# Kernel tuning notes

Hardware: AMD Instinct MI355X
Metric: run time of the kernel (lower is better)

Reference implementation:

```python
import jax, jax.numpy as jnp
import numpy as np

BS, SEQ, NV, DM, K = 128, 2048, 64, 512, 64
MAX_ITER, TOL = 10, 1e-4


def setup_inputs() -> dict:
    key = jax.random.key(0)
    k1, k2, k3, k4 = jax.random.split(key, 4)
    x = jax.random.normal(k1, (BS, SEQ, NV), jnp.float32)
    bound = 1.0 / np.sqrt(SEQ)
    W = jax.random.uniform(k2, (DM, SEQ), jnp.float32, -bound, bound)  # nn.Linear weight
    b = jax.random.uniform(k3, (DM,), jnp.float32, -bound, bound)
    centroids = jax.random.normal(k4, (K, DM), jnp.float32)  # kaiming-uniform-init param (random stand-in)
    return {"x": x, "W": W, "b": b, "centroids": centroids}


def _kmeans(x_emb, centroids):
    # x_emb: [N, DM]; fixed-length scan with a `done` flag emulating torch's tol break.
    N = x_emb.shape[0]
    x_sq = jnp.sum(x_emb * x_emb, axis=1, keepdims=True)  # [N,1]

    def body(state, _):
        cent, ids, done = state
        # squared euclidean distances (argmin-equivalent to cdist p=2)
        d2 = x_sq - 2.0 * (x_emb @ cent.T) + jnp.sum(cent * cent, axis=1)  # [N,K]
        new_ids = jnp.argmin(d2, axis=1)
        sums = jax.ops.segment_sum(x_emb, new_ids, num_segments=K)          # [K,DM]
        counts = jax.ops.segment_sum(jnp.ones((N,), x_emb.dtype), new_ids, num_segments=K)
        means = sums / jnp.maximum(counts, 1.0)[:, None]
        new_cent = jnp.where((counts > 0)[:, None], means, cent)  # empty cluster keeps old centroid
        shift = jnp.linalg.norm(new_cent - cent)
        cent_out = jnp.where(done, cent, new_cent)
        ids_out = jnp.where(done, ids, new_ids)
        done_out = done | (shift < TOL)
        return (cent_out, ids_out, done_out), None

    init = (centroids, jnp.zeros((N,), jnp.int32), jnp.array(False))
    (cent, ids, _), _ = jax.lax.scan(body, init, None, length=MAX_ITER)
    return ids, cent


def reference(x, W, b, centroids):
    # x: [bs, seq, n_vars] -> permute -> linear(seq->d_model) -> [bs*n_vars, d_model]
    xt = jnp.transpose(x, (0, 2, 1))                 # [bs, n_vars, seq]
    x_emb = (xt @ W.T + b).reshape(-1, DM)           # [bs*n_vars, d_model]
    ids, cent = _kmeans(x_emb, centroids)
    prob = jax.nn.one_hot(ids, K, dtype=jnp.float32).reshape(BS, NV, K)
    return prob, cent, x_emb
```

## Files before the change

### kernel.cpp

```cpp
#include <hip/hip_runtime.h>

#define SEQ 2048
#define NVAR 64
#define DMODEL 512
#define BSZ 128
#define KC 64
#define NPT (BSZ*NVAR)
#define MAXIT 10

typedef __bf16 bf16x8 __attribute__((ext_vector_type(8)));
typedef float f32x4 __attribute__((ext_vector_type(4)));

__device__ __forceinline__ void load_lds16(const void* g, void* l) {
  __builtin_amdgcn_global_load_lds((const __attribute__((address_space(1))) void*)g,
                                   (__attribute__((address_space(3))) void*)l, 16, 0, 0);
}

__device__ __forceinline__ unsigned short bf16_rn(float x) {
  unsigned int u = __float_as_uint(x);
  u += 0x7fffu + ((u >> 16) & 1u);
  return (unsigned short)(u >> 16);
}

__global__ __launch_bounds__(256) void init_k(const float* __restrict__ c0,
    float* __restrict__ cent, unsigned short* __restrict__ centh,
    unsigned short* __restrict__ centl, float* __restrict__ csq4,
    int* __restrict__ done, float* __restrict__ shift2, int* __restrict__ ticket) {
  const int k = blockIdx.x, t = threadIdx.x;
  __shared__ float red[256];
  float v0, v1;
  {
    int d = t;
    v0 = c0[k * DMODEL + d];
    cent[k * DMODEL + d] = v0;
    unsigned short h = bf16_rn(v0);
    centh[k * DMODEL + d] = h;
    centl[k * DMODEL + d] = bf16_rn(v0 - __uint_as_float((unsigned)h << 16));
  }
  {
    int d = t + 256;
    v1 = c0[k * DMODEL + d];
    cent[k * DMODEL + d] = v1;
    unsigned short h = bf16_rn(v1);
    centh[k * DMODEL + d] = h;
    centl[k * DMODEL + d] = bf16_rn(v1 - __uint_as_float((unsigned)h << 16));
  }
  red[t] = v0 * v0; __syncthreads();
  for (int s = 64; s > 0; s >>= 1) { if ((t & 127) < s) red[t] += red[t + s]; __syncthreads(); }
  if (t == 0)   csq4[0 * KC + k] = red[0];
  if (t == 128) csq4[1 * KC + k] = red[128];
  __syncthreads();
  red[t] = v1 * v1; __syncthreads();
  for (int s = 64; s > 0; s >>= 1) { if ((t & 127) < s) red[t] += red[t + s]; __syncthreads(); }
  if (t == 0)   csq4[2 * KC + k] = red[0];
  if (t == 128) csq4[3 * KC + k] = red[128];
  if (k == 0 && t < MAXIT) { shift2[t] = 0.f; ticket[t] = 0; }
  if (k == 0 && t == 31) *done = 0;
}

__global__ __launch_bounds__(256) void conv_w(const float* __restrict__ W,
    unsigned short* __restrict__ Wh, unsigned short* __restrict__ Wl) {
  int i = (blockIdx.x * 256 + threadIdx.x) * 4;
  float4 v = *(const float4*)(W + i);
  ushort4 h, l;
  h.x = bf16_rn(v.x); l.x = bf16_rn(v.x - __uint_as_float((unsigned)h.x << 16));
  h.y = bf16_rn(v.y); l.y = bf16_rn(v.y - __uint_as_float((unsigned)h.y << 16));
  h.z = bf16_rn(v.z); l.z = bf16_rn(v.z - __uint_as_float((unsigned)h.z << 16));
  h.w = bf16_rn(v.w); l.w = bf16_rn(v.w - __uint_as_float((unsigned)h.w << 16));
  *(ushort4*)(Wh + i) = h;
  *(ushort4*)(Wl + i) = l;
}

__global__ __launch_bounds__(256) void conv_x(const float* __restrict__ x,
    unsigned short* __restrict__ Xh, unsigned short* __restrict__ Xl) {
  __shared__ float tile[64 * 65];
  const int k0 = blockIdx.x * 64;
  const int bs = blockIdx.y;
  const int t = threadIdx.x;
  const float* xb = x + (size_t)bs * SEQ * NVAR + (size_t)k0 * NVAR;
  #pragma unroll
  for (int p = 0; p < 4; ++p) {
    int idx = t + 256 * p;
    int row = idx >> 4, c4 = (idx & 15) * 4;
    float4 v = *(const float4*)(xb + row * NVAR + c4);
    tile[row * 65 + c4 + 0] = v.x; tile[row * 65 + c4 + 1] = v.y;
    tile[row * 65 + c4 + 2] = v.z; tile[row * 65 + c4 + 3] = v.w;
  }
  __syncthreads();
  const int v = t >> 2;
  const int kc = (t & 3) * 16;
  unsigned short h[16], l[16];
  #pragma unroll
  for (int j = 0; j < 16; ++j) {
    float f = tile[(kc + j) * 65 + v];
    h[j] = bf16_rn(f);
    l[j] = bf16_rn(f - __uint_as_float((unsigned)h[j] << 16));
  }
  size_t off = (size_t)(bs * 64 + v) * SEQ + k0 + kc;
  *(uint4*)(Xh + off)     = *(uint4*)&h[0];
  *(uint4*)(Xh + off + 8) = *(uint4*)&h[8];
  *(uint4*)(Xl + off)     = *(uint4*)&l[0];
  *(uint4*)(Xl + off + 8) = *(uint4*)&l[8];
}

__global__ __launch_bounds__(256) void gemm_mfma(
    const unsigned short* __restrict__ Ah, const unsigned short* __restrict__ Al,
    const unsigned short* __restrict__ Bh, const unsigned short* __restrict__ Bl,
    const float* __restrict__ bias, float* __restrict__ emb) {
  __shared__ unsigned short sAh[32 * 64] __attribute__((aligned(16)));
  __shared__ unsigned short sAl[32 * 64] __attribute__((aligned(16)));
  __shared__ unsigned short sBh[256 * 64] __attribute__((aligned(16)));
  __shared__ unsigned short sBl[256 * 64] __attribute__((aligned(16)));
  const int t = threadIdx.x;
  const int w = t >> 6, lane = t & 63;
  const int m0 = blockIdx.x * 32;
  const int n0 = blockIdx.y * 256;
  const int wn = w * 64;
  const int lrow = lane >> 3, sl8 = lane & 7;
  const int csrc = sl8 ^ lrow;

  f32x4 acc[2][4];
  #pragma unroll
  for (int i = 0; i < 2; ++i)
    #pragma unroll
    for (int j = 0; j < 4; ++j) acc[i][j] = (f32x4){0.f, 0.f, 0.f, 0.f};

  for (int kt = 0; kt < SEQ; kt += 64) {
    __syncthreads();
    {
      const int r = w * 8 + lrow;
      const size_t ga = (size_t)(m0 + r) * SEQ + kt + csrc * 8;
      load_lds16(Ah + ga, &sAh[r * 64 + sl8 * 8]);
      load_lds16(Al + ga, &sAl[r * 64 + sl8 * 8]);
    }
    #pragma unroll
    for (int i = 0; i < 8; ++i) {
      const int r = w * 64 + i * 8 + lrow;
      const size_t gb = (size_t)(n0 + r) * SEQ + kt + csrc * 8;
      load_lds16(Bh + gb, &sBh[r * 64 + sl8 * 8]);
      load_lds16(Bl + gb, &sBl[r * 64 + sl8 * 8]);
    }
    __syncthreads();
    #pragma unroll
    for (int kk = 0; kk < 2; ++kk) {
      const int sl = ((kk * 4 + (lane >> 4)) ^ (lane & 7)) * 8;
      bf16x8 ah[2], al[2], bh[4], bl[4];
      #pragma unroll
      for (int mi = 0; mi < 2; ++mi) {
        int off = (mi * 16 + (lane & 15)) * 64 + sl;
        ah[mi] = *(const bf16x8*)&sAh[off];
        al[mi] = *(const bf16x8*)&sAl[off];
      }
      #pragma unroll
      for (int ni = 0; ni < 4; ++ni) {
        int off = (wn + ni * 16 + (lane & 15)) * 64 + sl;
        bh[ni] = *(const bf16x8*)&sBh[off];
        bl[ni] = *(const bf16x8*)&sBl[off];
      }
      #pragma unroll
      for (int mi = 0; mi < 2; ++mi)
        #pragma unroll
        for (int ni = 0; ni < 4; ++ni) {
          acc[mi][ni] = __builtin_amdgcn_mfma_f32_16x16x32_bf16(ah[mi], bh[ni], acc[mi][ni], 0, 0, 0);
          acc[mi][ni] = __builtin_amdgcn_mfma_f32_16x16x32_bf16(ah[mi], bl[ni], acc[mi][ni], 0, 0, 0);
          acc[mi][ni] = __builtin_amdgcn_mfma_f32_16x16x32_bf16(al[mi], bh[ni], acc[mi][ni], 0, 0, 0);
        }
    }
  }
  #pragma unroll
  for (int ni = 0; ni < 4; ++ni) {
    const int n = n0 + wn + ni * 16 + (lane & 15);
    const float bv = bias[n];
    #pragma unroll
    for (int mi = 0; mi < 2; ++mi) {
      const int m = m0 + mi * 16 + (lane >> 4) * 4;
      #pragma unroll
      for (int r = 0; r < 4; ++r)
        emb[(size_t)(m + r) * DMODEL + n] = acc[mi][ni][r] + bv;
    }
  }
}

__global__ __launch_bounds__(256) void gemm_emb(const float* __restrict__ x,
    const float* __restrict__ W, const float* __restrict__ bias,
    float* __restrict__ emb) {
  __shared__ float As[64][64];
  __shared__ float Ws[64][132];
  const int bs = blockIdx.y;
  const int n0 = blockIdx.x * 128;
  const int t = threadIdx.x;
  const int tx = t & 15, ty = t >> 4;
  float bv[8];
  #pragma unroll
  for (int j = 0; j < 8; ++j) bv[j] = bias[n0 + 8 * tx + j];
  float acc[4][8];
  #pragma unroll
  for (int i = 0; i < 4; ++i)
    #pragma unroll
    for (int j = 0; j < 8; ++j) acc[i][j] = 0.f;
  const float* xb = x + (size_t)bs * SEQ * NVAR;
  for (int k0 = 0; k0 < SEQ; k0 += 64) {
    __syncthreads();
    {
      const float4* src = (const float4*)(xb + (size_t)k0 * NVAR);
      float4* dst = (float4*)&As[0][0];
      #pragma unroll
      for (int r = 0; r < 4; ++r) dst[t + 256 * r] = src[t + 256 * r];
    }
    #pragma unroll
    for (int r = 0; r < 8; ++r) {
      int idx = t + 256 * r;
      int k4 = idx & 15, n = idx >> 4;
      float4 wv = *(const float4*)(W + (size_t)(n0 + n) * SEQ + k0 + 4 * k4);
      Ws[4 * k4 + 0][n] = wv.x; Ws[4 * k4 + 1][n] = wv.y;
      Ws[4 * k4 + 2][n] = wv.z; Ws[4 * k4 + 3][n] = wv.w;
    }
    __syncthreads();
    #pragma unroll 8
    for (int kk = 0; kk < 64; ++kk) {
      const float4 a  = *(const float4*)&As[kk][4 * ty];
      const float4 w0 = *(const float4*)&Ws[kk][8 * tx];
      const float4 w1 = *(const float4*)&Ws[kk][8 * tx + 4];
      const float av[4] = {a.x, a.y, a.z, a.w};
      const float wv[8] = {w0.x, w0.y, w0.z, w0.w, w1.x, w1.y, w1.z, w1.w};
      #pragma unroll
      for (int i = 0; i < 4; ++i)
        #pragma unroll
        for (int j = 0; j < 8; ++j)
          acc[i][j] = fmaf(av[i], wv[j], acc[i][j]);
    }
  }
  #pragma unroll
  for (int i = 0; i < 4; ++i) {
    int row = bs * NVAR + 4 * ty + i;
    float4 o0 = make_float4(acc[i][0] + bv[0], acc[i][1] + bv[1],
                            acc[i][2] + bv[2], acc[i][3] + bv[3]);
    float4 o1 = make_float4(acc[i][4] + bv[4], acc[i][5] + bv[5],
                            acc[i][6] + bv[6], acc[i][7] + bv[7]);
    *(float4*)(emb + (size_t)row * DMODEL + n0 + 8 * tx) = o0;
    *(float4*)(emb + (size_t)row * DMODEL + n0 + 8 * tx + 4) = o1;
  }
}

__global__ __launch_bounds__(256) void conv_et(const float* __restrict__ emb,
    unsigned short* __restrict__ Eh, unsigned short* __restrict__ El,
    unsigned short* __restrict__ Eth, unsigned short* __restrict__ Etl) {
  __shared__ unsigned short Lh[64][72];
  __shared__ unsigned short Ll[64][72];
  const int d0 = blockIdx.x * 64;
  const int p0 = blockIdx.y * 64;
  const int t = threadIdx.x;
  #pragma unroll
  for (int q = 0; q < 2; ++q) {
    int idx = t + 256 * q;
    int r = idx >> 3, c = idx & 7;
    const float* src = emb + (size_t)(p0 + r) * DMODEL + d0 + c * 8;
    float4 v0 = *(const float4*)src;
    float4 v1 = *(const float4*)(src + 4);
    unsigned short h[8], l[8];
    const float vv[8] = {v0.x, v0.y, v0.z, v0.w, v1.x, v1.y, v1.z, v1.w};
    #pragma unroll
    for (int j = 0; j < 8; ++j) {
      h[j] = bf16_rn(vv[j]);
      l[j] = bf16_rn(vv[j] - __uint_as_float((unsigned)h[j] << 16));
    }
    size_t eo = (size_t)(p0 + r) * DMODEL + d0 + c * 8;
    *(uint4*)(Eh + eo) = *(uint4*)&h[0];
    *(uint4*)(El + eo) = *(uint4*)&l[0];
    *(uint4*)&Lh[r][c * 8] = *(uint4*)&h[0];
    *(uint4*)&Ll[r][c * 8] = *(uint4*)&l[0];
  }
  __syncthreads();
  #pragma unroll
  for (int q = 0; q < 2; ++q) {
    int idx = t + 256 * q;
    int dd = idx >> 3, pc = idx & 7;
    unsigned short h[8], l[8];
    #pragma unroll
    for (int j = 0; j < 8; ++j) {
      h[j] = Lh[pc * 8 + j][dd];
      l[j] = Ll[pc * 8 + j][dd];
    }
    size_t to = (size_t)(d0 + dd) * NPT + p0 + pc * 8;
    *(uint4*)(Eth + to) = *(uint4*)&h[0];
    *(uint4*)(Etl + to) = *(uint4*)&l[0];
  }
}

__global__ __launch_bounds__(256) void k12_fused(
    const unsigned short* __restrict__ Eh, const unsigned short* __restrict__ El,
    const unsigned short* __restrict__ Eth, const unsigned short* __restrict__ Etl,
    const unsigned short* __restrict__ Ch, const unsigned short* __restrict__ Cl,
    const float* __restrict__ csq4, const int* __restrict__ done,
    int* __restrict__ ids, float* __restrict__ pcnt, float* __restrict__ psum) {
  if (*done) return;
  __shared__ __align__(16) unsigned char smem[50176];
  __shared__ float csq_l[64];
  __shared__ int cnt_l[64];
  __shared__ int ids_l[128];
  const int t = threadIdx.x;
  const int w = t >> 6, lane = t & 63;
  const int g = blockIdx.x & 63, dq = blockIdx.x >> 6;
  const int p0 = g * 128;
  const int lrow = lane >> 3, sl8 = lane & 7;
  const int csrc = sl8 ^ lrow;

  {
    unsigned short* sEh = (unsigned short*)smem;
    unsigned short* sEl = (unsigned short*)(smem + 16384);
    unsigned short* sCh = (unsigned short*)(smem + 32768);
    unsigned short* sCl = (unsigned short*)(smem + 40960);
    if (t < 64) {
      csq_l[t] = csq4[t] + csq4[KC + t] + csq4[2 * KC + t] + csq4[3 * KC + t];
      cnt_l[t] = 0;
    }
    f32x4 acc[2][4];
    #pragma unroll
    for (int i = 0; i < 2; ++i)
      #pragma unroll
      for (int j = 0; j < 4; ++j) acc[i][j] = (f32x4){0.f, 0.f, 0.f, 0.f};

    for (int kt = 0; kt < DMODEL; kt += 64) {
      __syncthreads();
      #pragma unroll
      for (int i = 0; i < 4; ++i) {
        const int r = w * 32 + i * 8 + lrow;
        const size_t ga = (size_t)(p0 + r) * DMODEL + kt + csrc * 8;
        load_lds16(Eh + ga, &sEh[r * 64 + sl8 * 8]);
        load_lds16(El + ga, &sEl[r * 64 + sl8 * 8]);
      }
      #pragma unroll
      for (int i = 0; i < 2; ++i) {
        const int r = w * 16 + i * 8 + lrow;
        const size_t gc = (size_t)r * DMODEL + kt + csrc * 8;
        load_lds16(Ch + gc, &sCh[r * 64 + sl8 * 8]);
        load_lds16(Cl + gc, &sCl[r * 64 + sl8 * 8]);
      }
      __syncthreads();
      #pragma unroll
      for (int kk = 0; kk < 2; ++kk) {
        const int sl = ((kk * 4 + (lane >> 4)) ^ (lane & 7)) * 8;
        bf16x8 eh[2], el[2], ch[4], cl[4];
        #pragma unroll
        for (int mi = 0; mi < 2; ++mi) {
          int off = (w * 32 + mi * 16 + (lane & 15)) * 64 + sl;
          eh[mi] = *(const bf16x8*)&sEh[off];
          el[mi] = *(const bf16x8*)&sEl[off];
        }
        #pragma unroll
        for (int ni = 0; ni < 4; ++ni) {
          int off = (ni * 16 + (lane & 15)) * 64 + sl;
          ch[ni] = *(const bf16x8*)&sCh[off];
          cl[ni] = *(const bf16x8*)&sCl[off];
        }
        #pragma unroll
        for (int mi = 0; mi < 2; ++mi)
          #pragma unroll
          for (int ni = 0; ni < 4; ++ni) {
            acc[mi][ni] = __builtin_amdgcn_mfma_f32_16x16x32_bf16(eh[mi], ch[ni], acc[mi][ni], 0, 0, 0);
            acc[mi][ni] = __builtin_amdgcn_mfma_f32_16x16x32_bf16(eh[mi], cl[ni], acc[mi][ni], 0, 0, 0);
            acc[mi][ni] = __builtin_amdgcn_mfma_f32_16x16x32_bf16(el[mi], ch[ni], acc[mi][ni], 0, 0, 0);
          }
      }
    }
    #pragma unroll
    for (int mi = 0; mi < 2; ++mi) {
      #pragma unroll
      for (int r = 0; r < 4; ++r) {
        float bv = csq_l[lane & 15] - 2.f * acc[mi][0][r];
        int bk = lane & 15;
        #pragma unroll
        for (int ni = 1; ni < 4; ++ni) {
          const int k = ni * 16 + (lane & 15);
          float v = csq_l[k] - 2.f * acc[mi][ni][r];
          if (v < bv) { bv = v; bk = k; }
        }
        #pragma unroll
        for (int m = 1; m < 16; m <<= 1) {
          float ov = __shfl_xor(bv, m, 64);
          int   ok = __shfl_xor(bk, m, 64);
          if (ov < bv || (ov == bv && ok < bk)) { bv = ov; bk = ok; }
        }
        if ((lane & 15) == 0) {
          const int p = w * 32 + mi * 16 + (lane >> 4) * 4 + r;
          ids_l[p] = bk;
          atomicAdd(&cnt_l[bk], 1);
        }
      }
    }
  }
  __syncthreads();
  if (dq == 0) {
    if (t < 128) ids[p0 + t] = ids_l[t];
    if (t < 64) pcnt[g * KC + t] = (float)cnt_l[t];
  }

  {
    unsigned short* sOH = (unsigned short*)smem;
    unsigned short* sTh = (unsigned short*)(smem + 17408);
    unsigned short* sTl = (unsigned short*)(smem + 33792);
    #pragma unroll
    for (int q = 0; q < 4; ++q) {
      int c = t * 4 + q;
      int cl = c >> 4, pc = c & 15;
      unsigned short v[8];
      #pragma unroll
      for (int j = 0; j < 8; ++j)
        v[j] = (ids_l[pc * 8 + j] == cl) ? (unsigned short)0x3F80 : (unsigned short)0;
      *(uint4*)&sOH[cl * 136 + pc * 8] = *(uint4*)&v[0];
    }

    f32x4 acc[4][2];
    #pragma unroll
    for (int i = 0; i < 4; ++i)
      #pragma unroll
      for (int j = 0; j < 2; ++j) acc[i][j] = (f32x4){0.f, 0.f, 0.f, 0.f};

    for (int kt = 0; kt < 2; ++kt) {
      __syncthreads();
      #pragma unroll
      for (int i = 0; i < 4; ++i) {
        const int rr = w * 32 + i * 8 + lrow;
        const size_t gt = (size_t)(dq * 128 + rr) * NPT + g * 128 + kt * 64 + csrc * 8;
        load_lds16(Eth + gt, &sTh[rr * 64 + sl8 * 8]);
        load_lds16(Etl + gt, &sTl[rr * 64 + sl8 * 8]);
      }
      __syncthreads();
      #pragma unroll
      for (int kk = 0; kk < 2; ++kk) {
        const int quad = lane >> 4;
        const int poff = kt * 64 + kk * 32 + quad * 8;
        bf16x8 a[4], bh[2], bl[2];
        #pragma unroll
        for (int mi = 0; mi < 4; ++mi)
          a[mi] = *(const bf16x8*)&sOH[(mi * 16 + (lane & 15)) * 136 + poff];
        const int sl = ((kk * 4 + quad) ^ (lane & 7)) * 8;
        #pragma unroll
        for (int ni = 0; ni < 2; ++ni) {
          int off = (w * 32 + ni * 16 + (lane & 15)) * 64 + sl;
          bh[ni] = *(const bf16x8*)&sTh[off];
          bl[ni] = *(const bf16x8*)&sTl[off];
        }
        #pragma unroll
        for (int mi = 0; mi < 4; ++mi)
          #pragma unroll
          for (int ni = 0; ni < 2; ++ni) {
            acc[mi][ni] = __builtin_amdgcn_mfma_f32_16x16x32_bf16(a[mi], bh[ni], acc[mi][ni], 0, 0, 0);
            acc[mi][ni] = __builtin_amdgcn_mfma_f32_16x16x32_bf16(a[mi], bl[ni], acc[mi][ni], 0, 0, 0);
          }
      }
    }
    #pragma unroll
    for (int mi = 0; mi < 4; ++mi)
      #pragma unroll
      for (int ni = 0; ni < 2; ++ni) {
        const int cl = mi * 16 + (lane >> 4) * 4;
        const int d = dq * 128 + w * 32 + ni * 16 + (lane & 15);
        #pragma unroll
        for (int r = 0; r < 4; ++r)
          psum[((size_t)g * KC + cl + r) * DMODEL + d] = acc[mi][ni][r];
      }
  }
}

__global__ __launch_bounds__(128) void k3_update(float* __restrict__ cent,
    unsigned short* __restrict__ centh, unsigned short* __restrict__ centl,
    const float* __restrict__ psum, const float* __restrict__ pcnt,
    int* __restrict__ done, float* __restrict__ csq4,
    float* __restrict__ shift2, int* __restrict__ ticket, int iter) {
  if (*done) return;
  const int bk = blockIdx.x & 63, dq = blockIdx.x >> 6;
  const int t = threadIdx.x;
  __shared__ float red[128];
  __shared__ float cnt_s;
  red[t] = (t < 64) ? pcnt[(size_t)t * KC + bk] : 0.f;
  __syncthreads();
  for (int s = 64; s > 0; s >>= 1) { if (t < s) red[t] += red[t + s]; __syncthreads(); }
  if (t == 0) cnt_s = red[0];
  __syncthreads();
  const float count = cnt_s;
  const int d = dq * 128 + t;
  float s = 0.f;
  for (int g = 0; g < 64; ++g)
    s += psum[((size_t)g * KC + bk) * DMODEL + d];
  float oldv = cent[bk * DMODEL + d];
  float newv = (count > 0.f) ? (s / fmaxf(count, 1.f)) : oldv;
  cent[bk * DMODEL + d] = newv;
  unsigned short h = bf16_rn(newv);
  centh[bk * DMODEL + d] = h;
  centl[bk * DMODEL + d] = bf16_rn(newv - __uint_as_float((unsigned)h << 16));
  float df = newv - oldv;
  red[t] = df * df; __syncthreads();
  for (int s2 = 64; s2 > 0; s2 >>= 1) { if (t < s2) red[t] += red[t + s2]; __syncthreads(); }
  float tot_sh = red[0]; __syncthreads();
  red[t] = newv * newv; __syncthreads();
  for (int s2 = 64; s2 > 0; s2 >>= 1) { if (t < s2) red[t] += red[t + s2]; __syncthreads(); }
  if (t == 0) {
    csq4[dq * KC + bk] = red[0];
    atomicAdd(shift2 + iter, tot_sh);
    __threadfence();
    int tk = atomicAdd(ticket + iter, 1);
    if (tk == 255) {
      float tot = atomicAdd(shift2 + iter, 0.f);
      if (sqrtf(tot) < 1e-4f) *done = 1;
    }
  }
}

__global__ __launch_bounds__(256) void finalize_k(const int* __restrict__ ids,
    const float* __restrict__ cent, float* __restrict__ out) {
  int t = blockIdx.x * 256 + threadIdx.x;
  if (t < NPT * KC) {
    int n = t >> 6, k = t & 63;
    out[t] = (ids[n] == k) ? 1.f : 0.f;
  } else {
    int i = t - NPT * KC;
    if (i < KC * DMODEL) out[NPT * KC + i] = cent[i];
  }
}

extern "C" void kernel_launch(void* const* d_in, const int* in_sizes, int n_in,
                              void* d_out, int out_size, void* d_ws, size_t ws_size,
                              hipStream_t stream) {
  const float* x    = (const float*)d_in[0];
  const float* W    = (const float*)d_in[1];
  const float* bias = (const float*)d_in[2];
  const float* c0   = (const float*)d_in[3];
  float* out = (float*)d_out;
  float* emb_out = out + NPT * KC + KC * DMODEL;

  char* ws = (char*)d_ws;
  unsigned short* Ehi  = (unsigned short*)(ws + 0);
  unsigned short* Elo  = (unsigned short*)(ws + 8388608);
  unsigned short* Eth  = (unsigned short*)(ws + 16777216);
  unsigned short* Etl  = (unsigned short*)(ws + 25165824);
  float* psum    = (float*)(ws + 33554432);
  float* cent    = (float*)(ws + 41943040);
  unsigned short* centh = (unsigned short*)(ws + 42074112);
  unsigned short* centl = (unsigned short*)(ws + 42139648);
  float* csq4    = (float*)(ws + 42205184);
  float* shift2  = (float*)(ws + 42206208);
  int*   ticket  = (int*)(ws + 42206272);
  int*   done_f  = (int*)(ws + 42206336);
  float* pcnt    = (float*)(ws + 42206400);
  int*   ids     = (int*)(ws + 42271936);
  unsigned short* Xh = (unsigned short*)(ws + 0);
  unsigned short* Xl = (unsigned short*)(ws + 33554432);
  unsigned short* Wh = (unsigned short*)(ws + 67108864);
  unsigned short* Wl = (unsigned short*)(ws + 69206016);
  const size_t need_fast = 71303168;
  (void)n_in; (void)in_sizes; (void)out_size;

  if (ws_size >= need_fast) {
    conv_w<<<1024, 256, 0, stream>>>(W, Wh, Wl);
    conv_x<<<dim3(32, BSZ), 256, 0, stream>>>(x, Xh, Xl);
    gemm_mfma<<<dim3(256, 2), 256, 0, stream>>>(Xh, Xl, Wh, Wl, bias, emb_out);
  } else {
    gemm_emb<<<dim3(4, BSZ), 256, 0, stream>>>(x, W, bias, emb_out);
  }
  init_k<<<KC, 256, 0, stream>>>(c0, cent, centh, centl, csq4, done_f, shift2, ticket);
  conv_et<<<dim3(8, 128), 256, 0, stream>>>(emb_out, Ehi, Elo, Eth, Etl);
  for (int it = 0; it < MAXIT; ++it) {
    k12_fused<<<256, 256, 0, stream>>>(Ehi, Elo, Eth, Etl, centh, centl,
                                       csq4, done_f, ids, pcnt, psum);
    k3_update<<<256, 128, 0, stream>>>(cent, centh, centl, psum, pcnt, done_f,
                                       csq4, shift2, ticket, it);
  }
  finalize_k<<<2176, 256, 0, stream>>>(ids, cent, out);
}
```

Before: 506.0 us.

## Double-buffer LDS tiles in fused k-means assign/accumulate kernel

Converts both GEMM phases of the fused assignment/segment-sum kernel to double-buffered LDS staging. The next tile's global-to-LDS loads are issued before computing on the current one, with explicit vmcnt waits and barriers replacing the per-tile __syncthreads pairs. The second phase prefetches both transposed-embedding tiles while the one-hot matrix is being built. LDS per block grows from about 50KB to 96KB, which can cut occupancy to one block per CU. The psum reduction loop in the update kernel is also unrolled.

```diff
diff --git a/kernel.cpp b/kernel.cpp
--- a/kernel.cpp
+++ b/kernel.cpp
@@ -294,7 +294,7 @@
     const float* __restrict__ csq4, const int* __restrict__ done,
     int* __restrict__ ids, float* __restrict__ pcnt, float* __restrict__ psum) {
   if (*done) return;
-  __shared__ __align__(16) unsigned char smem[50176];
+  __shared__ __align__(16) unsigned char smem[98304];
   __shared__ float csq_l[64];
   __shared__ int cnt_l[64];
   __shared__ int ids_l[128];
@@ -305,87 +305,113 @@
   const int lrow = lane >> 3, sl8 = lane & 7;
   const int csrc = sl8 ^ lrow;
 
-  {
-    unsigned short* sEh = (unsigned short*)smem;
-    unsigned short* sEl = (unsigned short*)(smem + 16384);
-    unsigned short* sCh = (unsigned short*)(smem + 32768);
-    unsigned short* sCl = (unsigned short*)(smem + 40960);
-    if (t < 64) {
-      csq_l[t] = csq4[t] + csq4[KC + t] + csq4[2 * KC + t] + csq4[3 * KC + t];
-      cnt_l[t] = 0;
-    }
-    f32x4 acc[2][4];
-    #pragma unroll
-    for (int i = 0; i < 2; ++i)
-      #pragma unroll
-      for (int j = 0; j < 4; ++j) acc[i][j] = (f32x4){0.f, 0.f, 0.f, 0.f};
-
-    for (int kt = 0; kt < DMODEL; kt += 64) {
-      __syncthreads();
-      #pragma unroll
-      for (int i = 0; i < 4; ++i) {
-        const int r = w * 32 + i * 8 + lrow;
-        const size_t ga = (size_t)(p0 + r) * DMODEL + kt + csrc * 8;
-        load_lds16(Eh + ga, &sEh[r * 64 + sl8 * 8]);
-        load_lds16(El + ga, &sEl[r * 64 + sl8 * 8]);
+  if (t < 64) {
+    csq_l[t] = csq4[t] + csq4[KC + t] + csq4[2 * KC + t] + csq4[3 * KC + t];
+    cnt_l[t] = 0;
+  }
+  __syncthreads();
+
+#define STAGE_A(B, KT) do { \
+    unsigned short* bEh = (unsigned short*)(smem + (B) * 49152); \
+    unsigned short* bEl = (unsigned short*)(smem + (B) * 49152 + 16384); \
+    unsigned short* bCh = (unsigned short*)(smem + (B) * 49152 + 32768); \
+    unsigned short* bCl = (unsigned short*)(smem + (B) * 49152 + 40960); \
+    _Pragma("unroll") \
+    for (int i_ = 0; i_ < 4; ++i_) { \
+      const int r_ = w * 32 + i_ * 8 + lrow; \
+      const size_t ga_ = (size_t)(p0 + r_) * DMODEL + (KT) + csrc * 8; \
+      load_lds16(Eh + ga_, &bEh[r_ * 64 + sl8 * 8]); \
+      load_lds16(El + ga_, &bEl[r_ * 64 + sl8 * 8]); \
+    } \
+    _Pragma("unroll") \
+    for (int i_ = 0; i_ < 2; ++i_) { \
+      const int r_ = w * 16 + i_ * 8 + lrow; \
+      const size_t gc_ = (size_t)r_ * DMODEL + (KT) + csrc * 8; \
+      load_lds16(Ch + gc_, &bCh[r_ * 64 + sl8 * 8]); \
+      load_lds16(Cl + gc_, &bCl[r_ * 64 + sl8 * 8]); \
+    } \
+  } while (0)
+
+#define COMPUTE_A(B) do { \
+    const unsigned short* bEh = (const unsigned short*)(smem + (B) * 49152); \
+    const unsigned short* bEl = (const unsigned short*)(smem + (B) * 49152 + 16384); \
+    const unsigned short* bCh = (const unsigned short*)(smem + (B) * 49152 + 32768); \
+    const unsigned short* bCl = (const unsigned short*)(smem + (B) * 49152 + 40960); \
+    _Pragma("unroll") \
+    for (int kk = 0; kk < 2; ++kk) { \
+      const int sl = ((kk * 4 + (lane >> 4)) ^ (lane & 7)) * 8; \
+      bf16x8 eh[2], el[2], ch[4], cl[4]; \
+      _Pragma("unroll") \
+      for (int mi = 0; mi < 2; ++mi) { \
+        int off = (w * 32 + mi * 16 + (lane & 15)) * 64 + sl; \
+        eh[mi] = *(const bf16x8*)&bEh[off]; \
+        el[mi] = *(const bf16x8*)&bEl[off]; \
+      } \
+      _Pragma("unroll") \
+      for (int ni = 0; ni < 4; ++ni) { \
+        int off = (ni * 16 + (lane & 15)) * 64 + sl; \
+        ch[ni] = *(const bf16x8*)&bCh[off]; \
+        cl[ni] = *(const bf16x8*)&bCl[off]; \
+      } \
+      _Pragma("unroll") \
+      for (int mi = 0; mi < 2; ++mi) \
+        _Pragma("unroll") \
+        for (int ni = 0; ni < 4; ++ni) { \
+          acc[mi][ni] = __builtin_amdgcn_mfma_f32_16x16x32_bf16(eh[mi], ch[ni], acc[mi][ni], 0, 0, 0); \
+          acc[mi][ni] = __builtin_amdgcn_mfma_f32_16x16x32_bf16(eh[mi], cl[ni], acc[mi][ni], 0, 0, 0); \
+          acc[mi][ni] = __builtin_amdgcn_mfma_f32_16x16x32_bf16(el[mi], ch[ni], acc[mi][ni], 0, 0, 0); \
+        } \
+    } \
+  } while (0)
+
+  f32x4 acc[2][4];
+  #pragma unroll
+  for (int i = 0; i < 2; ++i)
+    #pragma unroll
+    for (int j = 0; j < 4; ++j) acc[i][j] = (f32x4){0.f, 0.f, 0.f, 0.f};
+
+  STAGE_A(0, 0);
+  for (int kt8 = 0; kt8 < 8; kt8 += 2) {
+    STAGE_A(1, (kt8 + 1) * 64);
+    asm volatile("s_waitcnt vmcnt(12)" ::: "memory");
+    __builtin_amdgcn_s_barrier();
+    __builtin_amdgcn_sched_barrier(0);
+    COMPUTE_A(0);
+    __builtin_amdgcn_s_barrier();
+    if (kt8 + 2 < 8) {
+      STAGE_A(0, (kt8 + 2) * 64);
+      asm volatile("s_waitcnt vmcnt(12)" ::: "memory");
+    } else {
+      asm volatile("s_waitcnt vmcnt(0)" ::: "memory");
+    }
+    __builtin_amdgcn_s_barrier();
+    __builtin_amdgcn_sched_barrier(0);
+    COMPUTE_A(1);
+    __builtin_amdgcn_s_barrier();
+  }
+
+  #pragma unroll
+  for (int mi = 0; mi < 2; ++mi) {
+    #pragma unroll
+    for (int r = 0; r < 4; ++r) {
+      float bv = csq_l[lane & 15] - 2.f * acc[mi][0][r];
+      int bk = lane & 15;
+      #pragma unroll
+      for (int ni = 1; ni < 4; ++ni) {
+        const int k = ni * 16 + (lane & 15);
+        float v = csq_l[k] - 2.f * acc[mi][ni][r];
+        if (v < bv) { bv = v; bk = k; }
       }
       #pragma unroll
-      for (int i = 0; i < 2; ++i) {
-        const int r = w * 16 + i * 8 + lrow;
-        const size_t gc = (size_t)r * DMODEL + kt + csrc * 8;
-        load_lds16(Ch + gc, &sCh[r * 64 + sl8 * 8]);
-        load_lds16(Cl + gc, &sCl[r * 64 + sl8 * 8]);
+      for (int m = 1; m < 16; m <<= 1) {
+        float ov = __shfl_xor(bv, m, 64);
+        int   ok = __shfl_xor(bk, m, 64);
+        if (ov < bv || (ov == bv && ok < bk)) { bv = ov; bk = ok; }
       }
-      __syncthreads();
-      #pragma unroll
-      for (int kk = 0; kk < 2; ++kk) {
-        const int sl = ((kk * 4 + (lane >> 4)) ^ (lane & 7)) * 8;
-        bf16x8 eh[2], el[2], ch[4], cl[4];
-        #pragma unroll
-        for (int mi = 0; mi < 2; ++mi) {
-          int off = (w * 32 + mi * 16 + (lane & 15)) * 64 + sl;
-          eh[mi] = *(const bf16x8*)&sEh[off];
-          el[mi] = *(const bf16x8*)&sEl[off];
-        }
-        #pragma unroll
-        for (int ni = 0; ni < 4; ++ni) {
-          int off = (ni * 16 + (lane & 15)) * 64 + sl;
-          ch[ni] = *(const bf16x8*)&sCh[off];
-          cl[ni] = *(const bf16x8*)&sCl[off];
-        }
-        #pragma unroll
-        for (int mi = 0; mi < 2; ++mi)
-          #pragma unroll
-          for (int ni = 0; ni < 4; ++ni) {
-            acc[mi][ni] = __builtin_amdgcn_mfma_f32_16x16x32_bf16(eh[mi], ch[ni], acc[mi][ni], 0, 0, 0);
-            acc[mi][ni] = __builtin_amdgcn_mfma_f32_16x16x32_bf16(eh[mi], cl[ni], acc[mi][ni], 0, 0, 0);
-            acc[mi][ni] = __builtin_amdgcn_mfma_f32_16x16x32_bf16(el[mi], ch[ni], acc[mi][ni], 0, 0, 0);
-          }
-      }
-    }
-    #pragma unroll
-    for (int mi = 0; mi < 2; ++mi) {
-      #pragma unroll
-      for (int r = 0; r < 4; ++r) {
-        float bv = csq_l[lane & 15] - 2.f * acc[mi][0][r];
-        int bk = lane & 15;
-        #pragma unroll
-        for (int ni = 1; ni < 4; ++ni) {
-          const int k = ni * 16 + (lane & 15);
-          float v = csq_l[k] - 2.f * acc[mi][ni][r];
-          if (v < bv) { bv = v; bk = k; }
-        }
-        #pragma unroll
-        for (int m = 1; m < 16; m <<= 1) {
-          float ov = __shfl_xor(bv, m, 64);
-          int   ok = __shfl_xor(bk, m, 64);
-          if (ov < bv || (ov == bv && ok < bk)) { bv = ov; bk = ok; }
-        }
-        if ((lane & 15) == 0) {
-          const int p = w * 32 + mi * 16 + (lane >> 4) * 4 + r;
-          ids_l[p] = bk;
-          atomicAdd(&cnt_l[bk], 1);
-        }
+      if ((lane & 15) == 0) {
+        const int p = w * 32 + mi * 16 + (lane >> 4) * 4 + r;
+        ids_l[p] = bk;
+        atomicAdd(&cnt_l[bk], 1);
       }
     }
   }
@@ -395,10 +421,49 @@
     if (t < 64) pcnt[g * KC + t] = (float)cnt_l[t];
   }
 
+#define STAGE_B(B, KT) do { \
+    unsigned short* bTh = (unsigned short*)(smem + 17408 + (B) * 32768); \
+    unsigned short* bTl = (unsigned short*)(smem + 17408 + (B) * 32768 + 16384); \
+    _Pragma("unroll") \
+    for (int i_ = 0; i_ < 4; ++i_) { \
+      const int rr_ = w * 32 + i_ * 8 + lrow; \
+      const size_t gt_ = (size_t)(dq * 128 + rr_) * NPT + g * 128 + (KT) + csrc * 8; \
+      load_lds16(Eth + gt_, &bTh[rr_ * 64 + sl8 * 8]); \
+      load_lds16(Etl + gt_, &bTl[rr_ * 64 + sl8 * 8]); \
+    } \
+  } while (0)
+
+#define COMPUTE_B(B, KT) do { \
+    const unsigned short* bTh = (const unsigned short*)(smem + 17408 + (B) * 32768); \
+    const unsigned short* bTl = (const unsigned short*)(smem + 17408 + (B) * 32768 + 16384); \
+    _Pragma("unroll") \
+    for (int kk = 0; kk < 2; ++kk) { \
+      const int quad = lane >> 4; \
+      const int poff = (KT) + kk * 32 + quad * 8; \
+      bf16x8 a[4], bh[2], bl[2]; \
+      _Pragma("unroll") \
+      for (int mi = 0; mi < 4; ++mi) \
+        a[mi] = *(const bf16x8*)&sOH[(mi * 16 + (lane & 15)) * 136 + poff]; \
+      const int sl = ((kk * 4 + quad) ^ (lane & 7)) * 8; \
+      _Pragma("unroll") \
+      for (int ni = 0; ni < 2; ++ni) { \
+        int off = (w * 32 + ni * 16 + (lane & 15)) * 64 + sl; \
+        bh[ni] = *(const bf16x8*)&bTh[off]; \
+        bl[ni] = *(const bf16x8*)&bTl[off]; \
+      } \
+      _Pragma("unroll") \
+      for (int mi = 0; mi < 4; ++mi) \
+        _Pragma("unroll") \
+        for (int ni = 0; ni < 2; ++ni) { \
+          bcc[mi][ni] = __builtin_amdgcn_mfma_f32_16x16x32_bf16(a[mi], bh[ni], bcc[mi][ni], 0, 0, 0); \
+          bcc[mi][ni] = __builtin_amdgcn_mfma_f32_16x16x32_bf16(a[mi], bl[ni], bcc[mi][ni], 0, 0, 0); \
+        } \
+    } \
+  } while (0)
+
   {
     unsigned short* sOH = (unsigned short*)smem;
-    unsigned short* sTh = (unsigned short*)(smem + 17408);
-    unsigned short* sTl = (unsigned short*)(smem + 33792);
+    STAGE_B(0, 0);
     #pragma unroll
     for (int q = 0; q < 4; ++q) {
       int c = t * 4 + q;
@@ -409,47 +474,24 @@
         v[j] = (ids_l[pc * 8 + j] == cl) ? (unsigned short)0x3F80 : (unsigned short)0;
       *(uint4*)&sOH[cl * 136 + pc * 8] = *(uint4*)&v[0];
     }
-
-    f32x4 acc[4][2];
+    STAGE_B(1, 64);
+
+    f32x4 bcc[4][2];
     #pragma unroll
     for (int i = 0; i < 4; ++i)
       #pragma unroll
-      for (int j = 0; j < 2; ++j) acc[i][j] = (f32x4){0.f, 0.f, 0.f, 0.f};
-
-    for (int kt = 0; kt < 2; ++kt) {
-      __syncthreads();
-      #pragma unroll
-      for (int i = 0; i < 4; ++i) {
-        const int rr = w * 32 + i * 8 + lrow;
-        const size_t gt = (size_t)(dq * 128 + rr) * NPT + g * 128 + kt * 64 + csrc * 8;
-        load_lds16(Eth + gt, &sTh[rr * 64 + sl8 * 8]);
-        load_lds16(Etl + gt, &sTl[rr * 64 + sl8 * 8]);
-      }
-      __syncthreads();
-      #pragma unroll
-      for (int kk = 0; kk < 2; ++kk) {
-        const int quad = lane >> 4;
-        const int poff = kt * 64 + kk * 32 + quad * 8;
-        bf16x8 a[4], bh[2], bl[2];
-        #pragma unroll
-        for (int mi = 0; mi < 4; ++mi)
-          a[mi] = *(const bf16x8*)&sOH[(mi * 16 + (lane & 15)) * 136 + poff];
-        const int sl = ((kk * 4 + quad) ^ (lane & 7)) * 8;
-        #pragma unroll
-        for (int ni = 0; ni < 2; ++ni) {
-          int off = (w * 32 + ni * 16 + (lane & 15)) * 64 + sl;
-          bh[ni] = *(const bf16x8*)&sTh[off];
-          bl[ni] = *(const bf16x8*)&sTl[off];
-        }
-        #pragma unroll
-        for (int mi = 0; mi < 4; ++mi)
-          #pragma unroll
-          for (int ni = 0; ni < 2; ++ni) {
-            acc[mi][ni] = __builtin_amdgcn_mfma_f32_16x16x32_bf16(a[mi], bh[ni], acc[mi][ni], 0, 0, 0);
-            acc[mi][ni] = __builtin_amdgcn_mfma_f32_16x16x32_bf16(a[mi], bl[ni], acc[mi][ni], 0, 0, 0);
-          }
-      }
-    }
+      for (int j = 0; j < 2; ++j) bcc[i][j] = (f32x4){0.f, 0.f, 0.f, 0.f};
+
+    asm volatile("s_waitcnt lgkmcnt(0)" ::: "memory");
+    asm volatile("s_waitcnt vmcnt(8)" ::: "memory");
+    __builtin_amdgcn_s_barrier();
+    __builtin_amdgcn_sched_barrier(0);
+    COMPUTE_B(0, 0);
+    asm volatile("s_waitcnt vmcnt(0)" ::: "memory");
+    __builtin_amdgcn_s_barrier();
+    __builtin_amdgcn_sched_barrier(0);
+    COMPUTE_B(1, 64);
+
     #pragma unroll
     for (int mi = 0; mi < 4; ++mi)
       #pragma unroll
@@ -458,9 +500,13 @@
         const int d = dq * 128 + w * 32 + ni * 16 + (lane & 15);
         #pragma unroll
         for (int r = 0; r < 4; ++r)
-          psum[((size_t)g * KC + cl + r) * DMODEL + d] = acc[mi][ni][r];
+          psum[((size_t)g * KC + cl + r) * DMODEL + d] = bcc[mi][ni][r];
       }
   }
+#undef STAGE_A
+#undef COMPUTE_A
+#undef STAGE_B
+#undef COMPUTE_B
 }
 
 __global__ __launch_bounds__(128) void k3_update(float* __restrict__ cent,
@@ -481,6 +527,7 @@
   const float count = cnt_s;
   const int d = dq * 128 + t;
   float s = 0.f;
+  #pragma unroll 16
   for (int g = 0; g < 64; ++g)
     s += psum[((size_t)g * KC + bk) * DMODEL + d];
   float oldv = cent[bk * DMODEL + d];
```

Measured after the change: 494.8 us. 2.2% less time.
